# Kernel tuning notes

Hardware: AMD Instinct MI355X
Metric: run time of the kernel (lower is better)

The kernel has to match this reference:

```python
import jax, jax.numpy as jnp
import numpy as np

D_MODEL = 1024
H = 16
D_HEAD = D_MODEL // H
EPS = 1e-5  # torch LayerNorm default


def setup_inputs() -> dict:
    key = jax.random.key(0)
    ks = jax.random.split(key, 10)
    bs, seq = 4, 2048
    scale = 1.0 / np.sqrt(D_MODEL)
    return {
        "q": jax.random.normal(ks[0], (bs, seq, D_MODEL), jnp.float32),
        "k": jax.random.normal(ks[1], (bs, seq, D_MODEL), jnp.float32),
        "v": jax.random.normal(ks[2], (bs, seq, D_MODEL), jnp.float32),
        "zero_mask": jnp.zeros((bs, 1, 1, seq), jnp.float32),
        "Wq": jax.random.normal(ks[3], (D_MODEL, D_MODEL), jnp.float32) * scale,
        "Wk": jax.random.normal(ks[4], (D_MODEL, D_MODEL), jnp.float32) * scale,
        "Wv": jax.random.normal(ks[5], (D_MODEL, D_MODEL), jnp.float32) * scale,
        "Wo": jax.random.normal(ks[6], (D_MODEL, D_MODEL), jnp.float32) * scale,
        "gamma": jnp.ones((D_MODEL,), jnp.float32),
        "beta": jnp.zeros((D_MODEL,), jnp.float32),
    }


def reference(q, k, v, zero_mask, Wq, Wk, Wv, Wo, gamma, beta):
    bs, seq_q, _ = q.shape
    seq_k = k.shape[1]
    residual = q
    # Projections (torch Linear: x @ W.T), split into heads -> (bs, h, seq, d)
    qh = (q @ Wq.T).reshape(bs, seq_q, H, D_HEAD).transpose(0, 2, 1, 3)
    kh = (k @ Wk.T).reshape(bs, seq_k, H, D_HEAD).transpose(0, 2, 1, 3)
    vh = (v @ Wv.T).reshape(bs, seq_k, H, D_HEAD).transpose(0, 2, 1, 3)
    # Scaled dot-product attention with additive -1e9 * zero_mask
    att = jnp.einsum("bhqd,bhkd->bhqk", qh, kh) / np.sqrt(D_HEAD)
    att = att + zero_mask * -1e9
    att = jax.nn.softmax(att, axis=-1)
    # dropout: identity in eval-mode reference
    ctx = jnp.einsum("bhqk,bhkd->bhqd", att, vh)
    ctx = ctx.transpose(0, 2, 1, 3).reshape(bs, seq_q, D_MODEL)
    out = ctx @ Wo.T
    out = out + residual
    # LayerNorm over last dim
    mu = jnp.mean(out, axis=-1, keepdims=True)
    var = jnp.var(out, axis=-1, keepdims=True)
    out = (out - mu) * jax.lax.rsqrt(var + EPS) * gamma + beta
    return out
```

## Files before the change

kernel.cpp:

```cpp
#include <hip/hip_runtime.h>

typedef __bf16 bf16x8 __attribute__((ext_vector_type(8)));
typedef float  f32x4  __attribute__((ext_vector_type(4)));
typedef short  s16x4  __attribute__((ext_vector_type(4)));

#define D_MODEL 1024
#define SEQ 2048
#define BS 4
#define NH 16
#define DH 64
#define MTOT (BS * SEQ)

#define AS1 __attribute__((address_space(1)))
#define AS3 __attribute__((address_space(3)))

template <typename T>
__device__ inline bf16x8 ld8(const T* p);

template <>
__device__ inline bf16x8 ld8<float>(const float* p) {
    f32x4 a = *(const f32x4*)p;
    f32x4 b = *(const f32x4*)(p + 4);
    bf16x8 r;
    r[0] = (__bf16)a[0]; r[1] = (__bf16)a[1]; r[2] = (__bf16)a[2]; r[3] = (__bf16)a[3];
    r[4] = (__bf16)b[0]; r[5] = (__bf16)b[1]; r[6] = (__bf16)b[2]; r[7] = (__bf16)b[3];
    return r;
}

template <>
__device__ inline bf16x8 ld8<__bf16>(const __bf16* p) {
    return *(const bf16x8*)p;
}

__global__ __launch_bounds__(256) void cvt4_kernel(
    const float* __restrict__ a, const float* __restrict__ b,
    const float* __restrict__ c, const float* __restrict__ e,
    __bf16* __restrict__ x, __bf16* __restrict__ y,
    __bf16* __restrict__ z, __bf16* __restrict__ w)
{
    const float* s = (blockIdx.y == 0) ? a : (blockIdx.y == 1) ? b : (blockIdx.y == 2) ? c : e;
    __bf16*      d = (blockIdx.y == 0) ? x : (blockIdx.y == 1) ? y : (blockIdx.y == 2) ? z : w;
    const long i = ((long)blockIdx.x * 256 + threadIdx.x) * 8;
    *(bf16x8*)(d + i) = ld8<float>(s + i);
}

__global__ __launch_bounds__(256) void gemm_qkv(
    const float* __restrict__ q, const float* __restrict__ k, const float* __restrict__ v,
    const __bf16* __restrict__ Wb,
    __bf16* __restrict__ Qp, __bf16* __restrict__ Kp, __bf16* __restrict__ Vp)
{
    __shared__ __align__(16) __bf16 As[128][48];
    __shared__ __align__(16) __bf16 Bs[128 * 32];
    const int K = D_MODEL, N = D_MODEL;
    const int z = blockIdx.z;
    const float* A = (z == 0) ? q : (z == 1) ? k : v;
    const __bf16* B = Wb + (long)z * D_MODEL * D_MODEL;
    __bf16* C = (z == 0) ? Qp : (z == 1) ? Kp : Vp;

    const int t = threadIdx.x;
    const int wave = t >> 6, lane = t & 63;
    const int quad = lane >> 4, l15 = lane & 15;
    const int wm = (wave >> 1) * 64, wn = (wave & 1) * 64;
    const long m0 = (long)blockIdx.x * 128;
    const long n0 = (long)blockIdx.y * 128;
    const int sr = t >> 2, sc = (t & 3) * 8;

    const __bf16* gB = B + (n0 + (t >> 2)) * (long)K + (t & 3) * 8;
    __bf16* lB0 = Bs + wave * 512;
    __bf16* lB1 = Bs + 2048 + wave * 512;

    f32x4 acc[4][4] = {};

    for (int k0 = 0; k0 < K; k0 += 32) {
        __builtin_amdgcn_global_load_lds((const AS1 void*)(gB + k0),          (AS3 void*)lB0, 16, 0, 0);
        __builtin_amdgcn_global_load_lds((const AS1 void*)(gB + 64 * K + k0), (AS3 void*)lB1, 16, 0, 0);
        *(bf16x8*)&As[sr][sc]      = ld8<float>(&A[(m0 + sr) * K + k0 + sc]);
        *(bf16x8*)&As[sr + 64][sc] = ld8<float>(&A[(m0 + sr + 64) * K + k0 + sc]);
        __syncthreads();
        bf16x8 af[4], bfr[4];
#pragma unroll
        for (int i = 0; i < 4; ++i) af[i]  = *(const bf16x8*)&As[wm + i * 16 + l15][quad * 8];
#pragma unroll
        for (int i = 0; i < 4; ++i) bfr[i] = *(const bf16x8*)&Bs[(wn + i * 16 + l15) * 32 + quad * 8];
#pragma unroll
        for (int i = 0; i < 4; ++i)
#pragma unroll
            for (int j = 0; j < 4; ++j)
                acc[i][j] = __builtin_amdgcn_mfma_f32_16x16x32_bf16(af[i], bfr[j], acc[i][j], 0, 0, 0);
        __syncthreads();
    }

#pragma unroll
    for (int i = 0; i < 4; ++i)
#pragma unroll
        for (int j = 0; j < 4; ++j) {
            const long r = m0 + wm + i * 16 + quad * 4;
            const long c = n0 + wn + j * 16 + l15;
#pragma unroll
            for (int reg = 0; reg < 4; ++reg)
                C[(r + reg) * N + c] = (__bf16)acc[i][j][reg];
        }
}

__global__ __launch_bounds__(256) void gemm_bb(
    const __bf16* __restrict__ A, const __bf16* __restrict__ B,
    __bf16* __restrict__ C, int M, int N, int K)
{
    __shared__ __align__(16) __bf16 As[128 * 32];
    __shared__ __align__(16) __bf16 Bs[128 * 32];
    const int t = threadIdx.x;
    const int wave = t >> 6, lane = t & 63;
    const int quad = lane >> 4, l15 = lane & 15;
    const int wm = (wave >> 1) * 64, wn = (wave & 1) * 64;
    const long m0 = (long)blockIdx.x * 128;
    const long n0 = (long)blockIdx.y * 128;

    const __bf16* gA = A + (m0 + (t >> 2)) * (long)K + (t & 3) * 8;
    const __bf16* gB = B + (n0 + (t >> 2)) * (long)K + (t & 3) * 8;
    __bf16* lA0 = As + wave * 512;
    __bf16* lA1 = As + 2048 + wave * 512;
    __bf16* lB0 = Bs + wave * 512;
    __bf16* lB1 = Bs + 2048 + wave * 512;

    f32x4 acc[4][4] = {};

    for (int k0 = 0; k0 < K; k0 += 32) {
        __builtin_amdgcn_global_load_lds((const AS1 void*)(gA + k0),          (AS3 void*)lA0, 16, 0, 0);
        __builtin_amdgcn_global_load_lds((const AS1 void*)(gA + 64 * K + k0), (AS3 void*)lA1, 16, 0, 0);
        __builtin_amdgcn_global_load_lds((const AS1 void*)(gB + k0),          (AS3 void*)lB0, 16, 0, 0);
        __builtin_amdgcn_global_load_lds((const AS1 void*)(gB + 64 * K + k0), (AS3 void*)lB1, 16, 0, 0);
        __syncthreads();
        bf16x8 af[4], bfr[4];
#pragma unroll
        for (int i = 0; i < 4; ++i) af[i]  = *(const bf16x8*)&As[(wm + i * 16 + l15) * 32 + quad * 8];
#pragma unroll
        for (int i = 0; i < 4; ++i) bfr[i] = *(const bf16x8*)&Bs[(wn + i * 16 + l15) * 32 + quad * 8];
#pragma unroll
        for (int i = 0; i < 4; ++i)
#pragma unroll
            for (int j = 0; j < 4; ++j)
                acc[i][j] = __builtin_amdgcn_mfma_f32_16x16x32_bf16(af[i], bfr[j], acc[i][j], 0, 0, 0);
        __syncthreads();
    }

#pragma unroll
    for (int i = 0; i < 4; ++i)
#pragma unroll
        for (int j = 0; j < 4; ++j) {
            const long r = m0 + wm + i * 16 + quad * 4;
            const long c = n0 + wn + j * 16 + l15;
#pragma unroll
            for (int reg = 0; reg < 4; ++reg)
                C[(r + reg) * N + c] = (__bf16)acc[i][j][reg];
        }
}

__global__ __launch_bounds__(256, 2) void attn_kernel(
    const __bf16* Qp, const __bf16* __restrict__ Kp, const __bf16* __restrict__ Vp,
    const float* __restrict__ mask, __bf16* Ctx)
{
    __shared__ __align__(16) __bf16 Ks[64][72];
    __shared__ __align__(16) __bf16 Vt[64][76];
    __shared__ __align__(16) float  Msk[SEQ];

    const int t = threadIdx.x;
    const int wave = t >> 6, lane = t & 63;
    const int quad = lane >> 4, l15 = lane & 15;
    const int qt = blockIdx.x;
    const int bh = blockIdx.y;
    const int b = bh >> 4, h = bh & 15;
    const long rowbase = (long)b * SEQ;
    const int q0 = qt * 256 + wave * 16;

    {
        const float C2 = -1e9f * 1.44269504f;
        f32x4 m0 = *(const f32x4*)&mask[rowbase + t * 8];
        f32x4 m1 = *(const f32x4*)&mask[rowbase + t * 8 + 4];
        f32x4 s0, s1;
#pragma unroll
        for (int e = 0; e < 4; ++e) { s0[e] = m0[e] * C2; s1[e] = m1[e] * C2; }
        *(f32x4*)&Msk[t * 8]     = s0;
        *(f32x4*)&Msk[t * 8 + 4] = s1;
    }

    bf16x8 aq[4][2];
#pragma unroll
    for (int qi = 0; qi < 4; ++qi) {
        const long qrow = rowbase + q0 + qi * 64 + l15;
        const __bf16* qptr = Qp + qrow * D_MODEL + h * DH + quad * 8;
        aq[qi][0] = *(const bf16x8*)(qptr);
        aq[qi][1] = *(const bf16x8*)(qptr + 32);
    }

    float l_acc[4] = {};
    f32x4 acc_o[4][4] = {};

    const int sr = t >> 2, sc = (t & 3) * 16;
    const int kp2 = (t >> 3) * 2, dc = (t & 7) * 8;
    const float C1 = 0.125f * 1.44269504f;

    for (int kt = 0; kt < SEQ / 64; ++kt) {
        __syncthreads();
        {
            const __bf16* kptr = Kp + (rowbase + kt * 64 + sr) * D_MODEL + h * DH + sc;
            *(bf16x8*)&Ks[sr][sc]     = *(const bf16x8*)(kptr);
            *(bf16x8*)&Ks[sr][sc + 8] = *(const bf16x8*)(kptr + 8);
            const __bf16* vptr = Vp + (rowbase + kt * 64 + kp2) * D_MODEL + h * DH + dc;
            bf16x8 v0 = *(const bf16x8*)(vptr);
            bf16x8 v1 = *(const bf16x8*)(vptr + D_MODEL);
#pragma unroll
            for (int e = 0; e < 8; ++e) {
                union { __bf16 h2[2]; unsigned u; } pk;
                pk.h2[0] = v0[e]; pk.h2[1] = v1[e];
                *(unsigned*)&Vt[dc + e][kp2] = pk.u;
            }
        }
        __syncthreads();

        bf16x8 kf[4][2];
#pragma unroll
        for (int nt = 0; nt < 4; ++nt)
#pragma unroll
            for (int ks = 0; ks < 2; ++ks)
                kf[nt][ks] = *(const bf16x8*)&Ks[nt * 16 + l15][ks * 32 + quad * 8];
        s16x4 vtf[4][4];
#pragma unroll
        for (int nt = 0; nt < 4; ++nt)
#pragma unroll
            for (int dt = 0; dt < 4; ++dt)
                vtf[nt][dt] = *(const s16x4*)&Vt[dt * 16 + l15][nt * 16 + quad * 4];
        f32x4 mv[4];
#pragma unroll
        for (int nt = 0; nt < 4; ++nt)
            mv[nt] = *(const f32x4*)&Msk[kt * 64 + nt * 16 + quad * 4];

#pragma unroll
        for (int qi = 0; qi < 4; ++qi) {
            f32x4 st[4] = {};
#pragma unroll
            for (int ks = 0; ks < 2; ++ks)
#pragma unroll
                for (int nt = 0; nt < 4; ++nt)
                    st[nt] = __builtin_amdgcn_mfma_f32_16x16x32_bf16(kf[nt][ks], aq[qi][ks], st[nt], 0, 0, 0);
            s16x4 pp[4];
#pragma unroll
            for (int nt = 0; nt < 4; ++nt) {
                union { __bf16 hh[4]; s16x4 s; } u;
#pragma unroll
                for (int reg = 0; reg < 4; ++reg) {
                    const float pv = exp2f(fmaf(st[nt][reg], C1, mv[nt][reg]));
                    l_acc[qi] += pv;
                    u.hh[reg] = (__bf16)pv;
                }
                pp[nt] = u.s;
            }
#pragma unroll
            for (int nt = 0; nt < 4; ++nt)
#pragma unroll
                for (int dt = 0; dt < 4; ++dt)
                    acc_o[qi][dt] = __builtin_amdgcn_mfma_f32_16x16x16bf16_1k(pp[nt], vtf[nt][dt], acc_o[qi][dt], 0, 0, 0);
        }
    }

#pragma unroll
    for (int qi = 0; qi < 4; ++qi) {
        float l = l_acc[qi];
        l += __shfl_xor(l, 16, 64);
        l += __shfl_xor(l, 32, 64);
        const float inv = 1.f / l;
        float invq[4];
#pragma unroll
        for (int reg = 0; reg < 4; ++reg)
            invq[reg] = __shfl(inv, quad * 4 + reg, 64);
#pragma unroll
        for (int dt = 0; dt < 4; ++dt)
#pragma unroll
            for (int reg = 0; reg < 4; ++reg) {
                const long row = rowbase + q0 + qi * 64 + quad * 4 + reg;
                Ctx[row * D_MODEL + h * DH + dt * 16 + l15] = (__bf16)(acc_o[qi][dt][reg] * invq[reg]);
            }
    }
}

__global__ __launch_bounds__(256) void ln_kernel(
    const __bf16* __restrict__ Y, const float* __restrict__ R,
    const float* __restrict__ gamma, const float* __restrict__ beta,
    float* __restrict__ Out)
{
    __shared__ float red[8];
    const long row = blockIdx.x;
    const int t = threadIdx.x;
    const int wave = t >> 6, lane = t & 63;
    float x[4];
    float s = 0.f, s2 = 0.f;
#pragma unroll
    for (int i = 0; i < 4; ++i) {
        const int idx = i * 256 + t;
        const float v = (float)Y[row * D_MODEL + idx] + R[row * D_MODEL + idx];
        x[i] = v; s += v; s2 += v * v;
    }
#pragma unroll
    for (int off = 32; off >= 1; off >>= 1) {
        s  += __shfl_xor(s, off, 64);
        s2 += __shfl_xor(s2, off, 64);
    }
    if (lane == 0) { red[wave] = s; red[4 + wave] = s2; }
    __syncthreads();
    s  = red[0] + red[1] + red[2] + red[3];
    s2 = red[4] + red[5] + red[6] + red[7];
    const float mu   = s * (1.f / 1024.f);
    const float var  = s2 * (1.f / 1024.f) - mu * mu;
    const float rstd = rsqrtf(var + 1e-5f);
#pragma unroll
    for (int i = 0; i < 4; ++i) {
        const int idx = i * 256 + t;
        Out[row * D_MODEL + idx] = (x[i] - mu) * rstd * gamma[idx] + beta[idx];
    }
}

extern "C" void kernel_launch(void* const* d_in, const int* in_sizes, int n_in,
                              void* d_out, int out_size, void* d_ws, size_t ws_size,
                              hipStream_t stream)
{
    const float* q     = (const float*)d_in[0];
    const float* k     = (const float*)d_in[1];
    const float* v     = (const float*)d_in[2];
    const float* mask  = (const float*)d_in[3];
    const float* Wq    = (const float*)d_in[4];
    const float* Wk    = (const float*)d_in[5];
    const float* Wv    = (const float*)d_in[6];
    const float* Wo    = (const float*)d_in[7];
    const float* gamma = (const float*)d_in[8];
    const float* beta  = (const float*)d_in[9];
    float* out = (float*)d_out;

    const long NACT = (long)MTOT * D_MODEL;
    const long NW   = (long)D_MODEL * D_MODEL;

    __bf16* Qp = (__bf16*)d_ws;
    __bf16* Kp = Qp + NACT;
    __bf16* Vp = (__bf16*)d_out;
    __bf16* Wb = Vp + NACT;
    __bf16 *Wqb = Wb, *Wkb = Wb + NW, *Wvb = Wb + 2 * NW, *Wob = Wb + 3 * NW;
    __bf16* Y = Kp;

    cvt4_kernel<<<dim3(NW / 2048, 4), 256, 0, stream>>>(Wq, Wk, Wv, Wo, Wqb, Wkb, Wvb, Wob);

    gemm_qkv<<<dim3(MTOT / 128, D_MODEL / 128, 3), 256, 0, stream>>>(q, k, v, Wqb, Qp, Kp, Vp);

    attn_kernel<<<dim3(SEQ / 256, BS * NH), 256, 0, stream>>>(Qp, Kp, Vp, mask, Qp);

    gemm_bb<<<dim3(MTOT / 128, D_MODEL / 128), 256, 0, stream>>>(Qp, Wob, Y, MTOT, D_MODEL, D_MODEL);

    ln_kernel<<<MTOT, 256, 0, stream>>>(Y, q, gamma, beta, out);
}
```

Before: 412.1 us.

## Double GEMM K-step to 64 and halve attention query tile per block

Both GEMM kernels now stage a 64-wide K slab per iteration in two 32-wide halves, which halves the number of barrier pairs and loop iterations per tile while doubling LDS use. The attention kernel processes 128 queries per block instead of 256, giving twice as many blocks and fewer registers per thread, and drops the min-blocks launch bound. It also loads 64 mask values per key tile instead of prescaling the whole row up front. The cost is re-reading K/V tiles from memory twice as often in attention, plus the larger GEMM LDS footprint, which may reduce occupancy.

```diff
diff --git a/kernel.cpp b/kernel.cpp
--- a/kernel.cpp
+++ b/kernel.cpp
@@ -49,8 +49,8 @@
     const __bf16* __restrict__ Wb,
     __bf16* __restrict__ Qp, __bf16* __restrict__ Kp, __bf16* __restrict__ Vp)
 {
-    __shared__ __align__(16) __bf16 As[128][48];
-    __shared__ __align__(16) __bf16 Bs[128 * 32];
+    __shared__ __align__(16) __bf16 As[2 * 4096];
+    __shared__ __align__(16) __bf16 Bs[2 * 4096];
     const int K = D_MODEL, N = D_MODEL;
     const int z = blockIdx.z;
     const float* A = (z == 0) ? q : (z == 1) ? k : v;
@@ -65,28 +65,37 @@
     const long n0 = (long)blockIdx.y * 128;
     const int sr = t >> 2, sc = (t & 3) * 8;
 
-    const __bf16* gB = B + (n0 + (t >> 2)) * (long)K + (t & 3) * 8;
+    const __bf16* gB = B + (n0 + sr) * (long)K + sc;
     __bf16* lB0 = Bs + wave * 512;
     __bf16* lB1 = Bs + 2048 + wave * 512;
+    __bf16* lB2 = Bs + 4096 + wave * 512;
+    __bf16* lB3 = Bs + 6144 + wave * 512;
 
     f32x4 acc[4][4] = {};
 
-    for (int k0 = 0; k0 < K; k0 += 32) {
-        __builtin_amdgcn_global_load_lds((const AS1 void*)(gB + k0),          (AS3 void*)lB0, 16, 0, 0);
-        __builtin_amdgcn_global_load_lds((const AS1 void*)(gB + 64 * K + k0), (AS3 void*)lB1, 16, 0, 0);
-        *(bf16x8*)&As[sr][sc]      = ld8<float>(&A[(m0 + sr) * K + k0 + sc]);
-        *(bf16x8*)&As[sr + 64][sc] = ld8<float>(&A[(m0 + sr + 64) * K + k0 + sc]);
-        __syncthreads();
-        bf16x8 af[4], bfr[4];
-#pragma unroll
-        for (int i = 0; i < 4; ++i) af[i]  = *(const bf16x8*)&As[wm + i * 16 + l15][quad * 8];
-#pragma unroll
-        for (int i = 0; i < 4; ++i) bfr[i] = *(const bf16x8*)&Bs[(wn + i * 16 + l15) * 32 + quad * 8];
-#pragma unroll
-        for (int i = 0; i < 4; ++i)
-#pragma unroll
-            for (int j = 0; j < 4; ++j)
-                acc[i][j] = __builtin_amdgcn_mfma_f32_16x16x32_bf16(af[i], bfr[j], acc[i][j], 0, 0, 0);
+    for (int k0 = 0; k0 < K; k0 += 64) {
+        __builtin_amdgcn_global_load_lds((const AS1 void*)(gB + k0),               (AS3 void*)lB0, 16, 0, 0);
+        __builtin_amdgcn_global_load_lds((const AS1 void*)(gB + 64 * K + k0),      (AS3 void*)lB1, 16, 0, 0);
+        __builtin_amdgcn_global_load_lds((const AS1 void*)(gB + k0 + 32),          (AS3 void*)lB2, 16, 0, 0);
+        __builtin_amdgcn_global_load_lds((const AS1 void*)(gB + 64 * K + k0 + 32), (AS3 void*)lB3, 16, 0, 0);
+        *(bf16x8*)&As[sr * 32 + sc]               = ld8<float>(&A[(m0 + sr) * K + k0 + sc]);
+        *(bf16x8*)&As[(sr + 64) * 32 + sc]        = ld8<float>(&A[(m0 + sr + 64) * K + k0 + sc]);
+        *(bf16x8*)&As[4096 + sr * 32 + sc]        = ld8<float>(&A[(m0 + sr) * K + k0 + 32 + sc]);
+        *(bf16x8*)&As[4096 + (sr + 64) * 32 + sc] = ld8<float>(&A[(m0 + sr + 64) * K + k0 + 32 + sc]);
+        __syncthreads();
+#pragma unroll
+        for (int p = 0; p < 2; ++p) {
+            bf16x8 af[4], bfr[4];
+#pragma unroll
+            for (int i = 0; i < 4; ++i) af[i]  = *(const bf16x8*)&As[p * 4096 + (wm + i * 16 + l15) * 32 + quad * 8];
+#pragma unroll
+            for (int i = 0; i < 4; ++i) bfr[i] = *(const bf16x8*)&Bs[p * 4096 + (wn + i * 16 + l15) * 32 + quad * 8];
+#pragma unroll
+            for (int i = 0; i < 4; ++i)
+#pragma unroll
+                for (int j = 0; j < 4; ++j)
+                    acc[i][j] = __builtin_amdgcn_mfma_f32_16x16x32_bf16(af[i], bfr[j], acc[i][j], 0, 0, 0);
+        }
         __syncthreads();
     }
 
@@ -106,40 +115,52 @@
     const __bf16* __restrict__ A, const __bf16* __restrict__ B,
     __bf16* __restrict__ C, int M, int N, int K)
 {
-    __shared__ __align__(16) __bf16 As[128 * 32];
-    __shared__ __align__(16) __bf16 Bs[128 * 32];
+    __shared__ __align__(16) __bf16 As[2 * 4096];
+    __shared__ __align__(16) __bf16 Bs[2 * 4096];
     const int t = threadIdx.x;
     const int wave = t >> 6, lane = t & 63;
     const int quad = lane >> 4, l15 = lane & 15;
     const int wm = (wave >> 1) * 64, wn = (wave & 1) * 64;
     const long m0 = (long)blockIdx.x * 128;
     const long n0 = (long)blockIdx.y * 128;
-
-    const __bf16* gA = A + (m0 + (t >> 2)) * (long)K + (t & 3) * 8;
-    const __bf16* gB = B + (n0 + (t >> 2)) * (long)K + (t & 3) * 8;
+    const int sr = t >> 2, sc = (t & 3) * 8;
+
+    const __bf16* gA = A + (m0 + sr) * (long)K + sc;
+    const __bf16* gB = B + (n0 + sr) * (long)K + sc;
     __bf16* lA0 = As + wave * 512;
     __bf16* lA1 = As + 2048 + wave * 512;
+    __bf16* lA2 = As + 4096 + wave * 512;
+    __bf16* lA3 = As + 6144 + wave * 512;
     __bf16* lB0 = Bs + wave * 512;
     __bf16* lB1 = Bs + 2048 + wave * 512;
+    __bf16* lB2 = Bs + 4096 + wave * 512;
+    __bf16* lB3 = Bs + 6144 + wave * 512;
 
     f32x4 acc[4][4] = {};
 
-    for (int k0 = 0; k0 < K; k0 += 32) {
-        __builtin_amdgcn_global_load_lds((const AS1 void*)(gA + k0),          (AS3 void*)lA0, 16, 0, 0);
-        __builtin_amdgcn_global_load_lds((const AS1 void*)(gA + 64 * K + k0), (AS3 void*)lA1, 16, 0, 0);
-        __builtin_amdgcn_global_load_lds((const AS1 void*)(gB + k0),          (AS3 void*)lB0, 16, 0, 0);
-        __builtin_amdgcn_global_load_lds((const AS1 void*)(gB + 64 * K + k0), (AS3 void*)lB1, 16, 0, 0);
-        __syncthreads();
-        bf16x8 af[4], bfr[4];
-#pragma unroll
-        for (int i = 0; i < 4; ++i) af[i]  = *(const bf16x8*)&As[(wm + i * 16 + l15) * 32 + quad * 8];
-#pragma unroll
-        for (int i = 0; i < 4; ++i) bfr[i] = *(const bf16x8*)&Bs[(wn + i * 16 + l15) * 32 + quad * 8];
-#pragma unroll
-        for (int i = 0; i < 4; ++i)
-#pragma unroll
-            for (int j = 0; j < 4; ++j)
-                acc[i][j] = __builtin_amdgcn_mfma_f32_16x16x32_bf16(af[i], bfr[j], acc[i][j], 0, 0, 0);
+    for (int k0 = 0; k0 < K; k0 += 64) {
+        __builtin_amdgcn_global_load_lds((const AS1 void*)(gA + k0),               (AS3 void*)lA0, 16, 0, 0);
+        __builtin_amdgcn_global_load_lds((const AS1 void*)(gA + 64 * K + k0),      (AS3 void*)lA1, 16, 0, 0);
+        __builtin_amdgcn_global_load_lds((const AS1 void*)(gA + k0 + 32),          (AS3 void*)lA2, 16, 0, 0);
+        __builtin_amdgcn_global_load_lds((const AS1 void*)(gA + 64 * K + k0 + 32), (AS3 void*)lA3, 16, 0, 0);
+        __builtin_amdgcn_global_load_lds((const AS1 void*)(gB + k0),               (AS3 void*)lB0, 16, 0, 0);
+        __builtin_amdgcn_global_load_lds((const AS1 void*)(gB + 64 * K + k0),      (AS3 void*)lB1, 16, 0, 0);
+        __builtin_amdgcn_global_load_lds((const AS1 void*)(gB + k0 + 32),          (AS3 void*)lB2, 16, 0, 0);
+        __builtin_amdgcn_global_load_lds((const AS1 void*)(gB + 64 * K + k0 + 32), (AS3 void*)lB3, 16, 0, 0);
+        __syncthreads();
+#pragma unroll
+        for (int p = 0; p < 2; ++p) {
+            bf16x8 af[4], bfr[4];
+#pragma unroll
+            for (int i = 0; i < 4; ++i) af[i]  = *(const bf16x8*)&As[p * 4096 + (wm + i * 16 + l15) * 32 + quad * 8];
+#pragma unroll
+            for (int i = 0; i < 4; ++i) bfr[i] = *(const bf16x8*)&Bs[p * 4096 + (wn + i * 16 + l15) * 32 + quad * 8];
+#pragma unroll
+            for (int i = 0; i < 4; ++i)
+#pragma unroll
+                for (int j = 0; j < 4; ++j)
+                    acc[i][j] = __builtin_amdgcn_mfma_f32_16x16x32_bf16(af[i], bfr[j], acc[i][j], 0, 0, 0);
+        }
         __syncthreads();
     }
 
@@ -155,13 +176,13 @@
         }
 }
 
-__global__ __launch_bounds__(256, 2) void attn_kernel(
+__global__ __launch_bounds__(256) void attn_kernel(
     const __bf16* Qp, const __bf16* __restrict__ Kp, const __bf16* __restrict__ Vp,
     const float* __restrict__ mask, __bf16* Ctx)
 {
     __shared__ __align__(16) __bf16 Ks[64][72];
     __shared__ __align__(16) __bf16 Vt[64][76];
-    __shared__ __align__(16) float  Msk[SEQ];
+    __shared__ __align__(16) float  Ms[64];
 
     const int t = threadIdx.x;
     const int wave = t >> 6, lane = t & 63;
@@ -170,34 +191,24 @@
     const int bh = blockIdx.y;
     const int b = bh >> 4, h = bh & 15;
     const long rowbase = (long)b * SEQ;
-    const int q0 = qt * 256 + wave * 16;
-
-    {
-        const float C2 = -1e9f * 1.44269504f;
-        f32x4 m0 = *(const f32x4*)&mask[rowbase + t * 8];
-        f32x4 m1 = *(const f32x4*)&mask[rowbase + t * 8 + 4];
-        f32x4 s0, s1;
-#pragma unroll
-        for (int e = 0; e < 4; ++e) { s0[e] = m0[e] * C2; s1[e] = m1[e] * C2; }
-        *(f32x4*)&Msk[t * 8]     = s0;
-        *(f32x4*)&Msk[t * 8 + 4] = s1;
-    }
-
-    bf16x8 aq[4][2];
-#pragma unroll
-    for (int qi = 0; qi < 4; ++qi) {
+    const int q0 = qt * 128 + wave * 16;
+
+    bf16x8 aq[2][2];
+#pragma unroll
+    for (int qi = 0; qi < 2; ++qi) {
         const long qrow = rowbase + q0 + qi * 64 + l15;
         const __bf16* qptr = Qp + qrow * D_MODEL + h * DH + quad * 8;
         aq[qi][0] = *(const bf16x8*)(qptr);
         aq[qi][1] = *(const bf16x8*)(qptr + 32);
     }
 
-    float l_acc[4] = {};
-    f32x4 acc_o[4][4] = {};
+    float l_acc[2] = {0.f, 0.f};
+    f32x4 acc_o[2][4] = {};
 
     const int sr = t >> 2, sc = (t & 3) * 16;
     const int kp2 = (t >> 3) * 2, dc = (t & 7) * 8;
     const float C1 = 0.125f * 1.44269504f;
+    const float C2 = -1e9f * 1.44269504f;
 
     for (int kt = 0; kt < SEQ / 64; ++kt) {
         __syncthreads();
@@ -214,6 +225,7 @@
                 pk.h2[0] = v0[e]; pk.h2[1] = v1[e];
                 *(unsigned*)&Vt[dc + e][kp2] = pk.u;
             }
+            if (t < 64) Ms[t] = mask[rowbase + kt * 64 + t] * C2;
         }
         __syncthreads();
 
@@ -232,10 +244,10 @@
         f32x4 mv[4];
 #pragma unroll
         for (int nt = 0; nt < 4; ++nt)
-            mv[nt] = *(const f32x4*)&Msk[kt * 64 + nt * 16 + quad * 4];
-
-#pragma unroll
-        for (int qi = 0; qi < 4; ++qi) {
+            mv[nt] = *(const f32x4*)&Ms[nt * 16 + quad * 4];
+
+#pragma unroll
+        for (int qi = 0; qi < 2; ++qi) {
             f32x4 st[4] = {};
 #pragma unroll
             for (int ks = 0; ks < 2; ++ks)
@@ -263,7 +275,7 @@
     }
 
 #pragma unroll
-    for (int qi = 0; qi < 4; ++qi) {
+    for (int qi = 0; qi < 2; ++qi) {
         float l = l_acc[qi];
         l += __shfl_xor(l, 16, 64);
         l += __shfl_xor(l, 32, 64);
@@ -348,7 +360,7 @@
 
     gemm_qkv<<<dim3(MTOT / 128, D_MODEL / 128, 3), 256, 0, stream>>>(q, k, v, Wqb, Qp, Kp, Vp);
 
-    attn_kernel<<<dim3(SEQ / 256, BS * NH), 256, 0, stream>>>(Qp, Kp, Vp, mask, Qp);
+    attn_kernel<<<dim3(SEQ / 128, BS * NH), 256, 0, stream>>>(Qp, Kp, Vp, mask, Qp);
 
     gemm_bb<<<dim3(MTOT / 128, D_MODEL / 128), 256, 0, stream>>>(Qp, Wob, Y, MTOT, D_MODEL, D_MODEL);
 
```

Result: faster. 396.8 us (-3.7%).
